# Optimization experiments

Measured on AMD Instinct MI355X. Metric: run time of the kernel, lower is better.

The kernel has to match this reference:

```python
import jax, jax.numpy as jnp
import numpy as np

N, E = 100000, 1280000
IN_D, FEAT, HID, OUT = 256, 64, 64, 64
NEG_SLOPE = 0.2


def _gat_conv(x, src, dst, w, a_s, a_d, b, n):
    # x: [N, in], w: [in, out], a_s/a_d/b: [out]; edges src->dst (messages flow to dst)
    h = x @ w                                   # [N, out]
    e = jax.nn.leaky_relu((h @ a_s)[src] + (h @ a_d)[dst], NEG_SLOPE)  # [E]
    m = jax.ops.segment_max(e, dst, num_segments=n)                     # scatter-softmax (stable)
    ex = jnp.exp(e - m[dst])
    den = jax.ops.segment_sum(ex, dst, num_segments=n)
    alpha = ex / (den[dst] + 1e-16)
    out = jax.ops.segment_sum(alpha[:, None] * h[src], dst, num_segments=n)
    return out + b


def setup_inputs() -> dict:
    key = jax.random.key(0)
    ks = jax.random.split(key, 16)
    rn = lambda k, shape, s=0.05: jax.random.normal(k, shape, jnp.float32) * s
    return {
        'x': jax.random.normal(ks[0], (N, IN_D), jnp.float32),
        'src': jax.random.randint(ks[1], (E,), 0, N),
        'dst': jax.random.randint(ks[2], (E,), 0, N),
        'lin_w': rn(ks[3], (IN_D, FEAT)), 'lin_b': jnp.zeros((FEAT,), jnp.float32),
        'w1': rn(ks[4], (FEAT, HID)), 'a1s': rn(ks[5], (HID,)), 'a1d': rn(ks[6], (HID,)), 'b1': jnp.zeros((HID,), jnp.float32),
        'w2': rn(ks[7], (HID, HID)), 'a2s': rn(ks[8], (HID,)), 'a2d': rn(ks[9], (HID,)), 'b2': jnp.zeros((HID,), jnp.float32),
        'w3': rn(ks[10], (HID, OUT)), 'a3s': rn(ks[11], (OUT,)), 'a3d': rn(ks[12], (OUT,)), 'b3': jnp.zeros((OUT,), jnp.float32),
    }


def reference(x, src, dst, lin_w, lin_b, w1, a1s, a1d, b1, w2, a2s, a2d, b2, w3, a3s, a3d, b3):
    n = x.shape[0]
    loop = jnp.arange(n, dtype=src.dtype)        # GATConv add_self_loops=True
    s = jnp.concatenate([src, loop])
    d = jnp.concatenate([dst, loop])
    h = x @ lin_w + lin_b                        # feature_pre linear
    h = jax.nn.relu(_gat_conv(h, s, d, w1, a1s, a1d, b1, n))  # dropout is identity in eval
    h = jax.nn.relu(_gat_conv(h, s, d, w2, a2s, a2d, b2, n))
    h = _gat_conv(h, s, d, w3, a3s, a3d, b3, n)
    norm = jnp.linalg.norm(h, axis=-1, keepdims=True)          # F.normalize(p=2, dim=-1)
    return h / jnp.maximum(norm, 1e-12)
```

## Files before the change

kernel.cpp:

```cpp
#include <hip/hip_runtime.h>


constexpr float NEG_SLOPE = 0.2f;
#define BKT_SHIFT 9
#define BKT_N     512
#define PCHUNK    2048

typedef __attribute__((ext_vector_type(8))) short bf16x8;
typedef __attribute__((ext_vector_type(4))) float f32x4;

__device__ inline ushort f2bf(float x) {
    union { float f; uint u; } v; v.f = x;
    return (ushort)((v.u + 0x7FFFu + ((v.u >> 16) & 1u)) >> 16);
}
__device__ inline void bf2f(uint u, float& lo, float& hi) {
    union { uint u; float f; } a, b;
    a.u = u << 16; b.u = u & 0xFFFF0000u;
    lo = a.f; hi = b.f;
}
__device__ inline uint pk(float a, float b) {
    return (uint)f2bf(a) | ((uint)f2bf(b) << 16);
}

__global__ __launch_bounds__(256) void prep_w(
    const float* __restrict__ lw, const float* __restrict__ w1,
    const float* __restrict__ w2, const float* __restrict__ w3,
    ushort* __restrict__ lwT, ushort* __restrict__ w1T,
    ushort* __restrict__ w2T, ushort* __restrict__ w3T)
{
    const int i = blockIdx.x * 256 + threadIdx.x;
    if (i < 64 * 256) {
        const int nn = i >> 8, k = i & 255;
        lwT[i] = f2bf(lw[k * 64 + nn]);
    } else {
        const int j = i - 64 * 256;
        if (j < 4096) {
            const int nn = j >> 6, k = j & 63;
            w1T[j] = f2bf(w1[k * 64 + nn]);
            w2T[j] = f2bf(w2[k * 64 + nn]);
            w3T[j] = f2bf(w3[k * 64 + nn]);
        }
    }
}

__global__ __launch_bounds__(256) void gemm_pre(
    const float* __restrict__ x, const ushort* __restrict__ lwT,
    const float* __restrict__ bias, ushort* __restrict__ C, int M)
{
    __shared__ __align__(16) ushort ctile[4][16][64];
    const int tid = threadIdx.x;
    const int w = tid >> 6, lane = tid & 63;
    const int rw0 = (blockIdx.x * 4 + w) * 16;
    if (rw0 >= M) return;
    const int c = lane & 15, q = lane >> 4;

    const float* ap = x + (size_t)(rw0 + c) * 256 + q * 8;
    float4 pv[16];
    #pragma unroll
    for (int s = 0; s < 8; ++s) {
        pv[2 * s]     = *(const float4*)(ap + s * 32);
        pv[2 * s + 1] = *(const float4*)(ap + s * 32 + 4);
    }

    f32x4 acc[4];
    #pragma unroll
    for (int t = 0; t < 4; ++t) acc[t] = (f32x4){0.f, 0.f, 0.f, 0.f};

    #pragma unroll
    for (int s = 0; s < 8; ++s) {
        const float4 p0 = pv[2 * s];
        const float4 p1 = pv[2 * s + 1];
        bf16x8 af;
        af[0] = (short)f2bf(p0.x); af[1] = (short)f2bf(p0.y);
        af[2] = (short)f2bf(p0.z); af[3] = (short)f2bf(p0.w);
        af[4] = (short)f2bf(p1.x); af[5] = (short)f2bf(p1.y);
        af[6] = (short)f2bf(p1.z); af[7] = (short)f2bf(p1.w);
        #pragma unroll
        for (int t = 0; t < 4; ++t) {
            const bf16x8 bf = *(const bf16x8*)(lwT + (size_t)(t * 16 + c) * 256 + s * 32 + q * 8);
            acc[t] = __builtin_amdgcn_mfma_f32_16x16x32_bf16(af, bf, acc[t], 0, 0, 0);
        }
    }

    #pragma unroll
    for (int t = 0; t < 4; ++t) {
        const float bv = bias[t * 16 + c];
        #pragma unroll
        for (int r = 0; r < 4; ++r)
            ctile[w][q * 4 + r][t * 16 + c] = f2bf(acc[t][r] + bv);
    }
    const int row = lane >> 2, eo = (lane & 3) * 16;
    const uint4 v0 = *(const uint4*)(&ctile[w][row][eo]);
    const uint4 v1 = *(const uint4*)(&ctile[w][row][eo + 8]);
    *(uint4*)(C + (size_t)(rw0 + row) * 64 + eo)     = v0;
    *(uint4*)(C + (size_t)(rw0 + row) * 64 + eo + 8) = v1;
}

__global__ __launch_bounds__(256) void gemm_layer(
    const ushort* __restrict__ A, const ushort* __restrict__ WT,
    const float* __restrict__ a_s, const float* __restrict__ a_d,
    ushort* __restrict__ C, float* __restrict__ hs, float* __restrict__ hd, int M)
{
    __shared__ __align__(16) ushort ctile[4][16][64];
    const int tid = threadIdx.x;
    const int w = tid >> 6, lane = tid & 63;
    const int rw0 = (blockIdx.x * 4 + w) * 16;
    if (rw0 >= M) return;
    const int c = lane & 15, q = lane >> 4;

    const ushort* ap = A + (size_t)(rw0 + c) * 64 + q * 8;
    const bf16x8 a0 = *(const bf16x8*)(ap);
    const bf16x8 a1 = *(const bf16x8*)(ap + 32);

    f32x4 acc[4];
    #pragma unroll
    for (int t = 0; t < 4; ++t) {
        const ushort* bp = WT + (size_t)(t * 16 + c) * 64 + q * 8;
        const bf16x8 b0 = *(const bf16x8*)(bp);
        const bf16x8 b1 = *(const bf16x8*)(bp + 32);
        f32x4 a = (f32x4){0.f, 0.f, 0.f, 0.f};
        a = __builtin_amdgcn_mfma_f32_16x16x32_bf16(a0, b0, a, 0, 0, 0);
        a = __builtin_amdgcn_mfma_f32_16x16x32_bf16(a1, b1, a, 0, 0, 0);
        acc[t] = a;
    }

    float ps[4] = {0.f, 0.f, 0.f, 0.f}, pd[4] = {0.f, 0.f, 0.f, 0.f};
    #pragma unroll
    for (int t = 0; t < 4; ++t) {
        const float as = a_s[t * 16 + c], ad = a_d[t * 16 + c];
        #pragma unroll
        for (int r = 0; r < 4; ++r) {
            ps[r] = fmaf(acc[t][r], as, ps[r]);
            pd[r] = fmaf(acc[t][r], ad, pd[r]);
        }
    }
    #pragma unroll
    for (int r = 0; r < 4; ++r) {
        #pragma unroll
        for (int off = 1; off < 16; off <<= 1) {
            ps[r] += __shfl_xor(ps[r], off);
            pd[r] += __shfl_xor(pd[r], off);
        }
    }
    if (c == 0) {
        #pragma unroll
        for (int r = 0; r < 4; ++r) {
            hs[rw0 + q * 4 + r] = ps[r];
            hd[rw0 + q * 4 + r] = pd[r];
        }
    }

    #pragma unroll
    for (int t = 0; t < 4; ++t)
        #pragma unroll
        for (int r = 0; r < 4; ++r)
            ctile[w][q * 4 + r][t * 16 + c] = f2bf(acc[t][r]);
    const int row = lane >> 2, eo = (lane & 3) * 16;
    const uint4 v0 = *(const uint4*)(&ctile[w][row][eo]);
    const uint4 v1 = *(const uint4*)(&ctile[w][row][eo + 8]);
    *(uint4*)(C + (size_t)(rw0 + row) * 64 + eo)     = v0;
    *(uint4*)(C + (size_t)(rw0 + row) * 64 + eo + 8) = v1;
}

__global__ __launch_bounds__(256) void edge_hist(
    const int* __restrict__ dst, int* __restrict__ cnt, int e)
{
    const int i = blockIdx.x * blockDim.x + threadIdx.x;
    if (i < e) atomicAdd(&cnt[dst[i]], 1);
}

__global__ __launch_bounds__(256) void scan1(
    const int* __restrict__ cnt, int* __restrict__ out,
    int* __restrict__ bsum, int n)
{
    __shared__ int wsum[4];
    const int tid  = threadIdx.x;
    const int lane = tid & 63;
    const int w    = tid >> 6;
    const int base = blockIdx.x * 1024;
    int vals[4];
    int tsum = 0;
    #pragma unroll
    for (int i = 0; i < 4; ++i) {
        const int idx = base + tid * 4 + i;
        vals[i] = (idx < n) ? cnt[idx] : 0;
        tsum += vals[i];
    }
    int x = tsum;
    #pragma unroll
    for (int off = 1; off < 64; off <<= 1) {
        const int y = __shfl_up(x, off);
        if (lane >= off) x += y;
    }
    if (lane == 63) wsum[w] = x;
    __syncthreads();
    int wofs = 0;
    for (int k = 0; k < w; ++k) wofs += wsum[k];
    int excl = wofs + x - tsum;
    #pragma unroll
    for (int i = 0; i < 4; ++i) {
        const int idx = base + tid * 4 + i;
        if (idx < n) out[idx] = excl;
        excl += vals[i];
    }
    if (tid == 255) bsum[blockIdx.x] = wofs + x;
}

__global__ __launch_bounds__(128) void scan2(int* __restrict__ b, int nb)
{
    __shared__ int wtot[2];
    const int tid = threadIdx.x;
    const int lane = tid & 63;
    const int w = tid >> 6;
    const int v = (tid < nb) ? b[tid] : 0;
    int x = v;
    #pragma unroll
    for (int off = 1; off < 64; off <<= 1) {
        const int y = __shfl_up(x, off);
        if (lane >= off) x += y;
    }
    if (lane == 63) wtot[w] = x;
    __syncthreads();
    const int add = (w == 1) ? wtot[0] : 0;
    if (tid < nb) b[tid] = add + x - v;
}

__global__ __launch_bounds__(256) void scan3(
    int* __restrict__ out, const int* __restrict__ bsum, int n, int total)
{
    const int idx = blockIdx.x * blockDim.x + threadIdx.x;
    if (idx < n) out[idx] += bsum[idx >> 10];
    if (idx == 0) out[n] = total;
}

__global__ __launch_bounds__(256) void cursor_init(
    const int* __restrict__ offs, int* __restrict__ gcur, int n, int nb)
{
    const int b = threadIdx.x;
    if (b < nb) gcur[b] = offs[min(b << BKT_SHIFT, n)];
}

__global__ __launch_bounds__(256) void edge_partition(
    const int* __restrict__ src, const int* __restrict__ dst,
    int* __restrict__ gcursor, int2* __restrict__ pairs, int e, int nb)
{
    __shared__ int2 stage[PCHUNK];
    __shared__ int lcnt[256];
    __shared__ int lstart[256];
    __shared__ int lfill[256];
    __shared__ int gbase[256];
    __shared__ int wsum[4];

    const int tid  = threadIdx.x;
    const int lane = tid & 63;
    const int w    = tid >> 6;
    const int base = blockIdx.x * PCHUNK;
    const int cnt_here = min(PCHUNK, e - base);

    lcnt[tid] = 0; lfill[tid] = 0;
    __syncthreads();

    for (int i = tid; i < cnt_here; i += 256)
        atomicAdd(&lcnt[dst[base + i] >> BKT_SHIFT], 1);
    __syncthreads();

    const int v = lcnt[tid];
    int x = v;
    #pragma unroll
    for (int off = 1; off < 64; off <<= 1) {
        const int y = __shfl_up(x, off);
        if (lane >= off) x += y;
    }
    if (lane == 63) wsum[w] = x;
    __syncthreads();
    int carry = 0;
    for (int k = 0; k < w; ++k) carry += wsum[k];
    lstart[tid] = carry + x - v;
    if (tid < nb && v > 0) gbase[tid] = atomicAdd(&gcursor[tid], v);
    __syncthreads();

    for (int i = tid; i < cnt_here; i += 256) {
        int2 it; it.x = src[base + i]; it.y = dst[base + i];
        const int b = it.y >> BKT_SHIFT;
        const int p = lstart[b] + atomicAdd(&lfill[b], 1);
        stage[p] = it;
    }
    __syncthreads();

    for (int s = tid; s < cnt_here; s += 256) {
        const int2 it = stage[s];
        const int b = it.y >> BKT_SHIFT;
        pairs[gbase[b] + (s - lstart[b])] = it;
    }
}

__global__ __launch_bounds__(256) void bucket_scatter(
    const int2* __restrict__ pairs, const int* __restrict__ offs,
    int* __restrict__ ssrc, int n)
{
    __shared__ int pos[BKT_N];
    const int node0 = blockIdx.x << BKT_SHIFT;
    const int node1 = min(n, node0 + BKT_N);
    const int tid = threadIdx.x;
    for (int i = tid; i < node1 - node0; i += 256) pos[i] = offs[node0 + i];
    __syncthreads();
    const int e0 = offs[node0];
    const int e1 = offs[node1];
    for (int j = e0 + tid; j < e1; j += 256) {
        const int2 it = pairs[j];
        const int p = atomicAdd(&pos[it.y - node0], 1);
        ssrc[p] = it.x;
    }
}

template <int MODE>
__global__ __launch_bounds__(256) void gat_agg(
    const ushort* __restrict__ hp, const float* __restrict__ hs,
    const float* __restrict__ hd, const int* __restrict__ offs,
    const int* __restrict__ ssrc, const float* __restrict__ bias,
    void* __restrict__ outv, int n)
{
    const int wid  = (blockIdx.x * blockDim.x + threadIdx.x) >> 6;
    const int lane = threadIdx.x & 63;
    if (wid >= n) return;
    const int sub = lane >> 3;
    const int f0  = (lane & 7) * 8;

    const float hdi = hd[wid];
    float den = 0.f;
    float acc[8] = {};

    if (sub == 0) {
        float e = hs[wid] + hdi;
        e = (e > 0.f) ? e : NEG_SLOPE * e;
        const float ex = __expf(e);
        const uint4 t = *(const uint4*)(hp + (size_t)wid * 64 + f0);
        float f[8];
        bf2f(t.x, f[0], f[1]); bf2f(t.y, f[2], f[3]);
        bf2f(t.z, f[4], f[5]); bf2f(t.w, f[6], f[7]);
        den = ex;
        #pragma unroll
        for (int i = 0; i < 8; ++i) acc[i] = ex * f[i];
    }

    const int start = offs[wid];
    const int end   = offs[wid + 1];
    #pragma unroll 2
    for (int j = start + sub; j < end; j += 8) {
        const int s = ssrc[j];
        float e2 = hs[s] + hdi;
        e2 = (e2 > 0.f) ? e2 : NEG_SLOPE * e2;
        const float ex2 = __expf(e2);
        const uint4 t = *(const uint4*)(hp + (size_t)s * 64 + f0);
        float f[8];
        bf2f(t.x, f[0], f[1]); bf2f(t.y, f[2], f[3]);
        bf2f(t.z, f[4], f[5]); bf2f(t.w, f[6], f[7]);
        den += ex2;
        #pragma unroll
        for (int i = 0; i < 8; ++i) acc[i] = fmaf(ex2, f[i], acc[i]);
    }

    #pragma unroll
    for (int off = 8; off < 64; off <<= 1) {
        den += __shfl_xor(den, off);
        #pragma unroll
        for (int i = 0; i < 8; ++i) acc[i] += __shfl_xor(acc[i], off);
    }

    const float4 bv0 = *(const float4*)(bias + f0);
    const float4 bv1 = *(const float4*)(bias + f0 + 4);
    const float bb[8] = {bv0.x, bv0.y, bv0.z, bv0.w, bv1.x, bv1.y, bv1.z, bv1.w};
    const float inv = 1.f / (den + 1e-16f);
    float v[8];
    #pragma unroll
    for (int i = 0; i < 8; ++i) v[i] = acc[i] * inv + bb[i];

    if (MODE == 0) {
        #pragma unroll
        for (int i = 0; i < 8; ++i) v[i] = fmaxf(v[i], 0.f);
        if (sub == 0) {
            uint4 o;
            o.x = pk(v[0], v[1]); o.y = pk(v[2], v[3]);
            o.z = pk(v[4], v[5]); o.w = pk(v[6], v[7]);
            *(uint4*)((ushort*)outv + (size_t)wid * 64 + f0) = o;
        }
    } else {
        float sq = 0.f;
        #pragma unroll
        for (int i = 0; i < 8; ++i) sq += v[i] * v[i];
        #pragma unroll
        for (int off = 1; off < 8; off <<= 1) sq += __shfl_xor(sq, off);
        const float s = 1.f / fmaxf(sqrtf(sq), 1e-12f);
        if (sub == 0) {
            float* op = (float*)outv + (size_t)wid * 64 + f0;
            float4 o0, o1;
            o0.x = v[0] * s; o0.y = v[1] * s; o0.z = v[2] * s; o0.w = v[3] * s;
            o1.x = v[4] * s; o1.y = v[5] * s; o1.z = v[6] * s; o1.w = v[7] * s;
            *(float4*)(op)     = o0;
            *(float4*)(op + 4) = o1;
        }
    }
}

extern "C" void kernel_launch(void* const* d_in, const int* in_sizes, int n_in,
                              void* d_out, int out_size, void* d_ws, size_t ws_size,
                              hipStream_t stream)
{
    const float* x     = (const float*)d_in[0];
    const int*   src   = (const int*)d_in[1];
    const int*   dst   = (const int*)d_in[2];
    const float* lin_w = (const float*)d_in[3];
    const float* lin_b = (const float*)d_in[4];
    const float* w1  = (const float*)d_in[5];
    const float* a1s = (const float*)d_in[6];
    const float* a1d = (const float*)d_in[7];
    const float* b1  = (const float*)d_in[8];
    const float* w2  = (const float*)d_in[9];
    const float* a2s = (const float*)d_in[10];
    const float* a2d = (const float*)d_in[11];
    const float* b2  = (const float*)d_in[12];
    const float* w3  = (const float*)d_in[13];
    const float* a3s = (const float*)d_in[14];
    const float* a3d = (const float*)d_in[15];
    const float* b3  = (const float*)d_in[16];

    const int n = in_sizes[0] / 256;
    const int E = in_sizes[1];
    const int nb = (n + BKT_N - 1) >> BKT_SHIFT;

    char* wsp = (char*)d_ws;
    auto alloc = [&](size_t bytes) -> void* {
        void* p = (void*)wsp;
        wsp += (bytes + 255) & ~(size_t)255;
        return p;
    };
    ushort* bufA = (ushort*)alloc((size_t)n * 64 * sizeof(ushort));
    ushort* bufB = (ushort*)alloc((size_t)n * 64 * sizeof(ushort));
    float*  hs   = (float*)alloc((size_t)n * sizeof(float));
    float*  hd   = (float*)alloc((size_t)n * sizeof(float));
    int*    offs = (int*)alloc((size_t)(n + 1) * sizeof(int));
    int*    cnt  = (int*)alloc((size_t)n * sizeof(int));
    int*    bsum = (int*)alloc(1024 * sizeof(int));
    int*    gcur = (int*)alloc(256 * sizeof(int));
    int*    ssrc = (int*)alloc((size_t)E * sizeof(int));
    int2*   pairs = (int2*)alloc((size_t)E * sizeof(int2));
    ushort* lwT = (ushort*)alloc(64 * 256 * sizeof(ushort));
    ushort* w1T = (ushort*)alloc(64 * 64 * sizeof(ushort));
    ushort* w2T = (ushort*)alloc(64 * 64 * sizeof(ushort));
    ushort* w3T = (ushort*)alloc(64 * 64 * sizeof(ushort));

    const int edgeBlocks = (E + 255) / 256;
    const int nodeWaveBlocks = (n + 3) / 4;
    const int gemmBlocks = (n + 63) / 64;
    const int nScanBlocks = (n + 1023) / 1024;
    const int partBlocks = (E + PCHUNK - 1) / PCHUNK;

    prep_w<<<(64 * 256 + 4096 + 255) / 256, 256, 0, stream>>>(
        lin_w, w1, w2, w3, lwT, w1T, w2T, w3T);
    hipMemsetAsync(cnt, 0, (size_t)n * sizeof(int), stream);
    edge_hist<<<edgeBlocks, 256, 0, stream>>>(dst, cnt, E);
    scan1<<<nScanBlocks, 256, 0, stream>>>(cnt, offs, bsum, n);
    scan2<<<1, 128, 0, stream>>>(bsum, nScanBlocks);
    scan3<<<(n + 255) / 256, 256, 0, stream>>>(offs, bsum, n, E);
    cursor_init<<<1, 256, 0, stream>>>(offs, gcur, n, nb);
    edge_partition<<<partBlocks, 256, 0, stream>>>(src, dst, gcur, pairs, E, nb);
    bucket_scatter<<<nb, 256, 0, stream>>>(pairs, offs, ssrc, n);

    gemm_pre<<<gemmBlocks, 256, 0, stream>>>(x, lwT, lin_b, bufA, n);

    gemm_layer<<<gemmBlocks, 256, 0, stream>>>(bufA, w1T, a1s, a1d, bufB, hs, hd, n);
    gat_agg<0><<<nodeWaveBlocks, 256, 0, stream>>>(bufB, hs, hd, offs, ssrc, b1, bufA, n);

    gemm_layer<<<gemmBlocks, 256, 0, stream>>>(bufA, w2T, a2s, a2d, bufB, hs, hd, n);
    gat_agg<0><<<nodeWaveBlocks, 256, 0, stream>>>(bufB, hs, hd, offs, ssrc, b2, bufA, n);

    gemm_layer<<<gemmBlocks, 256, 0, stream>>>(bufA, w3T, a3s, a3d, bufB, hs, hd, n);
    gat_agg<1><<<nodeWaveBlocks, 256, 0, stream>>>(bufB, hs, hd, offs, ssrc, b3,
                                                   d_out, n);
}
```

Baseline: 493.4 us.

## Fuse preprocessing launches, pack edge pairs, and software-pipeline GAT aggregation loads

The memset is folded into prep_w, and scan2 becomes a last-block step inside scan1 driven by a ticket counter. cursor_init is dropped by having scan3 write the bucket cursors, so fewer small kernels are launched. Edge pairs are packed into one 32-bit word (local dst in the high bits, src in the low 17 bits), halving the pair traffic in partition and scatter. edge_hist reads four dst values per thread with a vector load. The aggregation loop now prefetches the next neighbor's index, score and features to hide gather latency. The packing only holds while n fits in 17 bits, and the ticket scan relies on threadfence ordering.

```diff
diff --git a/kernel.cpp b/kernel.cpp
--- a/kernel.cpp
+++ b/kernel.cpp
@@ -5,6 +5,7 @@
 #define BKT_SHIFT 9
 #define BKT_N     512
 #define PCHUNK    2048
+#define SRC_BITS  17
 
 typedef __attribute__((ext_vector_type(8))) short bf16x8;
 typedef __attribute__((ext_vector_type(4))) float f32x4;
@@ -26,9 +27,12 @@
     const float* __restrict__ lw, const float* __restrict__ w1,
     const float* __restrict__ w2, const float* __restrict__ w3,
     ushort* __restrict__ lwT, ushort* __restrict__ w1T,
-    ushort* __restrict__ w2T, ushort* __restrict__ w3T)
+    ushort* __restrict__ w2T, ushort* __restrict__ w3T,
+    int* __restrict__ cnt, int* __restrict__ ticket, int n)
 {
     const int i = blockIdx.x * 256 + threadIdx.x;
+    if (i < n) cnt[i] = 0;
+    if (i == 0) *ticket = 0;
     if (i < 64 * 256) {
         const int nn = i >> 8, k = i & 255;
         lwT[i] = f2bf(lw[k * 64 + nn]);
@@ -165,15 +169,22 @@
 __global__ __launch_bounds__(256) void edge_hist(
     const int* __restrict__ dst, int* __restrict__ cnt, int e)
 {
-    const int i = blockIdx.x * blockDim.x + threadIdx.x;
-    if (i < e) atomicAdd(&cnt[dst[i]], 1);
+    const int i0 = (blockIdx.x * 256 + threadIdx.x) * 4;
+    if (i0 + 3 < e) {
+        const int4 d = *(const int4*)(dst + i0);
+        atomicAdd(&cnt[d.x], 1); atomicAdd(&cnt[d.y], 1);
+        atomicAdd(&cnt[d.z], 1); atomicAdd(&cnt[d.w], 1);
+    } else {
+        for (int k = i0; k < e; ++k) atomicAdd(&cnt[dst[k]], 1);
+    }
 }
 
 __global__ __launch_bounds__(256) void scan1(
     const int* __restrict__ cnt, int* __restrict__ out,
-    int* __restrict__ bsum, int n)
+    int* __restrict__ bsum, int* __restrict__ ticket, int n, int nblk)
 {
     __shared__ int wsum[4];
+    __shared__ int amLastS;
     const int tid  = threadIdx.x;
     const int lane = tid & 63;
     const int w    = tid >> 6;
@@ -203,48 +214,48 @@
         if (idx < n) out[idx] = excl;
         excl += vals[i];
     }
-    if (tid == 255) bsum[blockIdx.x] = wofs + x;
-}
-
-__global__ __launch_bounds__(128) void scan2(int* __restrict__ b, int nb)
-{
-    __shared__ int wtot[2];
-    const int tid = threadIdx.x;
-    const int lane = tid & 63;
-    const int w = tid >> 6;
-    const int v = (tid < nb) ? b[tid] : 0;
-    int x = v;
-    #pragma unroll
-    for (int off = 1; off < 64; off <<= 1) {
-        const int y = __shfl_up(x, off);
-        if (lane >= off) x += y;
-    }
-    if (lane == 63) wtot[w] = x;
-    __syncthreads();
-    const int add = (w == 1) ? wtot[0] : 0;
-    if (tid < nb) b[tid] = add + x - v;
+    if (tid == 255) {
+        bsum[blockIdx.x] = wofs + x;
+        __threadfence();
+        amLastS = (atomicAdd(ticket, 1) == nblk - 1) ? 1 : 0;
+    }
+    __syncthreads();
+    if (amLastS) {
+        __threadfence();
+        const int v2 = (tid < nblk) ? bsum[tid] : 0;
+        int x2 = v2;
+        #pragma unroll
+        for (int off = 1; off < 64; off <<= 1) {
+            const int y = __shfl_up(x2, off);
+            if (lane >= off) x2 += y;
+        }
+        if (lane == 63) wsum[w] = x2;
+        __syncthreads();
+        int c2 = 0;
+        for (int k = 0; k < w; ++k) c2 += wsum[k];
+        if (tid < nblk) bsum[tid] = c2 + x2 - v2;
+    }
 }
 
 __global__ __launch_bounds__(256) void scan3(
-    int* __restrict__ out, const int* __restrict__ bsum, int n, int total)
+    int* __restrict__ out, const int* __restrict__ bsum,
+    int* __restrict__ gcur, int n, int total)
 {
     const int idx = blockIdx.x * blockDim.x + threadIdx.x;
-    if (idx < n) out[idx] += bsum[idx >> 10];
+    if (idx < n) {
+        const int v = out[idx] + bsum[idx >> 10];
+        out[idx] = v;
+        if ((idx & (BKT_N - 1)) == 0) gcur[idx >> BKT_SHIFT] = v;
+    }
     if (idx == 0) out[n] = total;
-}
-
-__global__ __launch_bounds__(256) void cursor_init(
-    const int* __restrict__ offs, int* __restrict__ gcur, int n, int nb)
-{
-    const int b = threadIdx.x;
-    if (b < nb) gcur[b] = offs[min(b << BKT_SHIFT, n)];
 }
 
 __global__ __launch_bounds__(256) void edge_partition(
     const int* __restrict__ src, const int* __restrict__ dst,
-    int* __restrict__ gcursor, int2* __restrict__ pairs, int e, int nb)
-{
-    __shared__ int2 stage[PCHUNK];
+    int* __restrict__ gcursor, int* __restrict__ pairs, int e, int nb)
+{
+    __shared__ int stage[PCHUNK];
+    __shared__ unsigned char sbkt[PCHUNK];
     __shared__ int lcnt[256];
     __shared__ int lstart[256];
     __shared__ int lfill[256];
@@ -280,22 +291,23 @@
     __syncthreads();
 
     for (int i = tid; i < cnt_here; i += 256) {
-        int2 it; it.x = src[base + i]; it.y = dst[base + i];
-        const int b = it.y >> BKT_SHIFT;
+        const int d = dst[base + i];
+        const int s = src[base + i];
+        const int b = d >> BKT_SHIFT;
         const int p = lstart[b] + atomicAdd(&lfill[b], 1);
-        stage[p] = it;
-    }
-    __syncthreads();
-
-    for (int s = tid; s < cnt_here; s += 256) {
-        const int2 it = stage[s];
-        const int b = it.y >> BKT_SHIFT;
-        pairs[gbase[b] + (s - lstart[b])] = it;
+        stage[p] = ((d & (BKT_N - 1)) << SRC_BITS) | s;
+        sbkt[p]  = (unsigned char)b;
+    }
+    __syncthreads();
+
+    for (int t = tid; t < cnt_here; t += 256) {
+        const int b = sbkt[t];
+        pairs[gbase[b] + (t - lstart[b])] = stage[t];
     }
 }
 
 __global__ __launch_bounds__(256) void bucket_scatter(
-    const int2* __restrict__ pairs, const int* __restrict__ offs,
+    const int* __restrict__ pairs, const int* __restrict__ offs,
     int* __restrict__ ssrc, int n)
 {
     __shared__ int pos[BKT_N];
@@ -307,9 +319,9 @@
     const int e0 = offs[node0];
     const int e1 = offs[node1];
     for (int j = e0 + tid; j < e1; j += 256) {
-        const int2 it = pairs[j];
-        const int p = atomicAdd(&pos[it.y - node0], 1);
-        ssrc[p] = it.x;
+        const int pr = pairs[j];
+        const int p = atomicAdd(&pos[pr >> SRC_BITS], 1);
+        ssrc[p] = pr & ((1 << SRC_BITS) - 1);
     }
 }
 
@@ -326,15 +338,24 @@
     const int sub = lane >> 3;
     const int f0  = (lane & 7) * 8;
 
+    const int start = offs[wid];
+    const int end   = offs[wid + 1];
     const float hdi = hd[wid];
+
+    int j = start + sub;
+    bool vC = j < end;
+    bool vN = j + 8 < end;
+    int sC = vC ? ssrc[j]     : wid;
+    int sN = vN ? ssrc[j + 8] : sC;
+
     float den = 0.f;
     float acc[8] = {};
 
     if (sub == 0) {
+        const uint4 t = *(const uint4*)(hp + (size_t)wid * 64 + f0);
         float e = hs[wid] + hdi;
         e = (e > 0.f) ? e : NEG_SLOPE * e;
         const float ex = __expf(e);
-        const uint4 t = *(const uint4*)(hp + (size_t)wid * 64 + f0);
         float f[8];
         bf2f(t.x, f[0], f[1]); bf2f(t.y, f[2], f[3]);
         bf2f(t.z, f[4], f[5]); bf2f(t.w, f[6], f[7]);
@@ -343,21 +364,27 @@
         for (int i = 0; i < 8; ++i) acc[i] = ex * f[i];
     }
 
-    const int start = offs[wid];
-    const int end   = offs[wid + 1];
-    #pragma unroll 2
-    for (int j = start + sub; j < end; j += 8) {
-        const int s = ssrc[j];
-        float e2 = hs[s] + hdi;
+    float hsC = hs[sC];
+    uint4 tC  = *(const uint4*)(hp + (size_t)sC * 64 + f0);
+
+    while (vC) {
+        const bool vNN = j + 16 < end;
+        const int  sNN = vNN ? ssrc[j + 16] : sN;
+        const float hsN = hs[sN];
+        const uint4 tN  = *(const uint4*)(hp + (size_t)sN * 64 + f0);
+
+        float e2 = hsC + hdi;
         e2 = (e2 > 0.f) ? e2 : NEG_SLOPE * e2;
         const float ex2 = __expf(e2);
-        const uint4 t = *(const uint4*)(hp + (size_t)s * 64 + f0);
         float f[8];
-        bf2f(t.x, f[0], f[1]); bf2f(t.y, f[2], f[3]);
-        bf2f(t.z, f[4], f[5]); bf2f(t.w, f[6], f[7]);
+        bf2f(tC.x, f[0], f[1]); bf2f(tC.y, f[2], f[3]);
+        bf2f(tC.z, f[4], f[5]); bf2f(tC.w, f[6], f[7]);
         den += ex2;
         #pragma unroll
         for (int i = 0; i < 8; ++i) acc[i] = fmaf(ex2, f[i], acc[i]);
+
+        vC = vN; vN = vNN; sC = sN; sN = sNN; hsC = hsN; tC = tN;
+        j += 8;
     }
 
     #pragma unroll
@@ -442,27 +469,25 @@
     int*    cnt  = (int*)alloc((size_t)n * sizeof(int));
     int*    bsum = (int*)alloc(1024 * sizeof(int));
     int*    gcur = (int*)alloc(256 * sizeof(int));
+    int*    tick = (int*)alloc(256 * sizeof(int));
     int*    ssrc = (int*)alloc((size_t)E * sizeof(int));
-    int2*   pairs = (int2*)alloc((size_t)E * sizeof(int2));
+    int*    pairs = (int*)alloc((size_t)E * sizeof(int));
     ushort* lwT = (ushort*)alloc(64 * 256 * sizeof(ushort));
     ushort* w1T = (ushort*)alloc(64 * 64 * sizeof(ushort));
     ushort* w2T = (ushort*)alloc(64 * 64 * sizeof(ushort));
     ushort* w3T = (ushort*)alloc(64 * 64 * sizeof(ushort));
 
-    const int edgeBlocks = (E + 255) / 256;
     const int nodeWaveBlocks = (n + 3) / 4;
     const int gemmBlocks = (n + 63) / 64;
     const int nScanBlocks = (n + 1023) / 1024;
     const int partBlocks = (E + PCHUNK - 1) / PCHUNK;
-
-    prep_w<<<(64 * 256 + 4096 + 255) / 256, 256, 0, stream>>>(
-        lin_w, w1, w2, w3, lwT, w1T, w2T, w3T);
-    hipMemsetAsync(cnt, 0, (size_t)n * sizeof(int), stream);
-    edge_hist<<<edgeBlocks, 256, 0, stream>>>(dst, cnt, E);
-    scan1<<<nScanBlocks, 256, 0, stream>>>(cnt, offs, bsum, n);
-    scan2<<<1, 128, 0, stream>>>(bsum, nScanBlocks);
-    scan3<<<(n + 255) / 256, 256, 0, stream>>>(offs, bsum, n, E);
-    cursor_init<<<1, 256, 0, stream>>>(offs, gcur, n, nb);
+    const int histBlocks = (E / 4 + 255) / 256 + 1;
+
+    prep_w<<<(n + 255) / 256, 256, 0, stream>>>(
+        lin_w, w1, w2, w3, lwT, w1T, w2T, w3T, cnt, tick, n);
+    edge_hist<<<histBlocks, 256, 0, stream>>>(dst, cnt, E);
+    scan1<<<nScanBlocks, 256, 0, stream>>>(cnt, offs, bsum, tick, n, nScanBlocks);
+    scan3<<<(n + 255) / 256, 256, 0, stream>>>(offs, bsum, gcur, n, E);
     edge_partition<<<partBlocks, 256, 0, stream>>>(src, dst, gcur, pairs, E, nb);
     bucket_scatter<<<nb, 256, 0, stream>>>(pairs, offs, ssrc, n);
 
```

After: 490.4 us. Within noise of the previous version (-0.6%).
